# Performance work log

Measured on AMD Instinct MI355X. Metric: run time of the kernel, lower is better.

The kernel has to match this reference:

```python
import jax, jax.numpy as jnp
import numpy as np

N = 20000
E = 320000
IN_C = 256
OUT_C = 64
HEADS = 4
NEG_SLOPE = 0.2
HID = HEADS * OUT_C  # 256, layer-2 input width (concat=True)


def setup_inputs() -> dict:
    key = jax.random.key(0)
    ks = jax.random.split(key, 16)
    x = jax.random.normal(ks[0], (N, IN_C), dtype=jnp.float32)
    edge_index = jax.random.randint(ks[1], (2, E), 0, N, dtype=jnp.int32)

    def glorot(k, shape, fan_in):
        return jax.random.normal(k, shape, dtype=jnp.float32) * np.float32(1.0 / np.sqrt(fan_in))

    inp = {"x": x, "edge_index": edge_index}
    # two GATv2Conv layers, both in_dim=256 -> heads*out=256
    for li, kbase in ((1, 2), (2, 9)):
        in_dim = IN_C if li == 1 else HID
        inp[f"Wl{li}"] = glorot(ks[kbase + 0], (in_dim, HID), in_dim)
        inp[f"bl{li}"] = jnp.zeros((HID,), jnp.float32)
        inp[f"Wr{li}"] = glorot(ks[kbase + 1], (in_dim, HID), in_dim)
        inp[f"br{li}"] = jnp.zeros((HID,), jnp.float32)
        inp[f"att{li}"] = glorot(ks[kbase + 2], (HEADS, OUT_C), OUT_C)
        inp[f"bias{li}"] = jnp.zeros((HID,), jnp.float32)
    return inp


def _gatv2_layer(x, src, dst, Wl, bl, Wr, br, att, bias):
    # GATv2Conv (PyG semantics, eval mode so attention dropout is identity)
    xl = (x @ Wl + bl).reshape(N, HEADS, OUT_C)  # source transform
    xr = (x @ Wr + br).reshape(N, HEADS, OUT_C)  # target transform
    # per-edge attention logits: a^T LeakyReLU(xl_j + xr_i)
    e = jax.nn.leaky_relu(xl[src] + xr[dst], NEG_SLOPE)      # [E2, H, C]
    logits = jnp.einsum('ehc,hc->eh', e, att)                # [E2, H]
    # segment softmax over incoming edges of each target node
    m = jax.ops.segment_max(logits, dst, num_segments=N)      # [N, H]
    ex = jnp.exp(logits - m[dst])
    denom = jax.ops.segment_sum(ex, dst, num_segments=N)      # [N, H]
    alpha = ex / denom[dst]                                   # [E2, H]
    msg = xl[src] * alpha[:, :, None]                         # [E2, H, C]
    out = jax.ops.segment_sum(msg, dst, num_segments=N)       # [N, H, C]
    return out.reshape(N, HID) + bias


def reference(x, edge_index, Wl1, bl1, Wr1, br1, att1, bias1,
              Wl2, bl2, Wr2, br2, att2, bias2):
    # add self loops (PyG GATv2Conv default add_self_loops=True)
    loops = jnp.arange(N, dtype=edge_index.dtype)
    src = jnp.concatenate([edge_index[0], loops])
    dst = jnp.concatenate([edge_index[1], loops])
    h = _gatv2_layer(x, src, dst, Wl1, bl1, Wr1, br1, att1, bias1)
    h = jax.nn.relu(h)
    h = _gatv2_layer(h, src, dst, Wl2, bl2, Wr2, br2, att2, bias2)
    h = jax.nn.relu(h)
    return h
```

## Files before the change

### kernel.cpp

```cpp
#include <hip/hip_runtime.h>

#define N_NODES 20000
#define E_EDGES 320000
#define E2 (E_EDGES + N_NODES)
#define HID 256
#define SLOPE 0.2f

typedef __bf16 bf16x8 __attribute__((ext_vector_type(8)));
typedef float  f32x4  __attribute__((ext_vector_type(4)));
typedef unsigned int uint4v __attribute__((ext_vector_type(4)));

__device__ __forceinline__ unsigned short f2bf(float f) {
    unsigned b = __float_as_uint(f);
    return (unsigned short)((b + 0x7FFFu + ((b >> 16) & 1u)) >> 16);
}
__device__ __forceinline__ float bf2f(unsigned short h) {
    return __uint_as_float(((unsigned)h) << 16);
}
__device__ __forceinline__ bf16x8 ld_frag(const unsigned short* p) {
    uint4v u = *reinterpret_cast<const uint4v*>(p);
    return __builtin_bit_cast(bf16x8, u);
}
#define MFMA16(a, b, c) __builtin_amdgcn_mfma_f32_16x16x32_bf16((a), (b), (c), 0, 0, 0)

__global__ __launch_bounds__(256) void k_init(int* __restrict__ deg, int* __restrict__ cursor) {
    int i = blockIdx.x * 256 + threadIdx.x;
    if (i < N_NODES) { deg[i] = 1; cursor[i] = 0; }
}

__global__ __launch_bounds__(256) void k_degree(const int* __restrict__ dst, int* __restrict__ deg) {
    int e = blockIdx.x * 256 + threadIdx.x;
    if (e < E_EDGES) atomicAdd(&deg[dst[e]], 1);
}

__global__ __launch_bounds__(1024) void k_scan(const int* __restrict__ deg, int* __restrict__ off) {
    __shared__ int wsum[16];
    const int tid  = threadIdx.x;
    const int wave = tid >> 6;
    const int lane = tid & 63;
    int carry = 0;
    for (int base = 0; base < N_NODES; base += 1024) {
        const int i = base + tid;
        const int v = (i < N_NODES) ? deg[i] : 0;
        int x = v;
        #pragma unroll
        for (int o = 1; o < 64; o <<= 1) {
            int t = __shfl_up(x, o);
            if (lane >= o) x += t;
        }
        if (lane == 63) wsum[wave] = x;
        __syncthreads();
        if (wave == 0 && lane < 16) {
            int y = wsum[lane];
            #pragma unroll
            for (int o = 1; o < 16; o <<= 1) {
                int t = __shfl_up(y, o);
                if (lane >= o) y += t;
            }
            wsum[lane] = y;
        }
        __syncthreads();
        const int wbase = (wave == 0) ? 0 : wsum[wave - 1];
        if (i < N_NODES) off[i] = carry + wbase + (x - v);
        carry += wsum[15];
        __syncthreads();
    }
    if (tid == 0) off[N_NODES] = carry;
}

__global__ __launch_bounds__(256) void k_fill(const int* __restrict__ srcA, const int* __restrict__ dstA,
                                              const int* __restrict__ off, int* __restrict__ cursor,
                                              int* __restrict__ csr_src) {
    int e = blockIdx.x * 256 + threadIdx.x;
    if (e >= E2) return;
    int s, d;
    if (e < E_EDGES) { s = srcA[e]; d = dstA[e]; }
    else             { s = d = e - E_EDGES; }
    int pos = atomicAdd(&cursor[d], 1);
    csr_src[off[d] + pos] = s;
}

__global__ __launch_bounds__(256) void k_cvt_x(const float* __restrict__ X,
                                               unsigned short* __restrict__ hi,
                                               unsigned short* __restrict__ lo) {
    const int i = blockIdx.x * 256 + threadIdx.x;
    if (i >= N_NODES * HID / 4) return;
    float4 v = ((const float4*)X)[i];
    ushort4 h, l;
    h.x = f2bf(v.x); l.x = f2bf(v.x - bf2f(h.x));
    h.y = f2bf(v.y); l.y = f2bf(v.y - bf2f(h.y));
    h.z = f2bf(v.z); l.z = f2bf(v.z - bf2f(h.z));
    h.w = f2bf(v.w); l.w = f2bf(v.w - bf2f(h.w));
    ((ushort4*)hi)[i] = h;
    ((ushort4*)lo)[i] = l;
}

__global__ __launch_bounds__(256) void k_cvt_w(const float* __restrict__ W0, const float* __restrict__ W1,
                                               const float* __restrict__ W2, const float* __restrict__ W3,
                                               unsigned short* __restrict__ wt_hi,
                                               unsigned short* __restrict__ wt_lo) {
    const float* W = (blockIdx.x == 0) ? W0 : (blockIdx.x == 1) ? W1 : (blockIdx.x == 2) ? W2 : W3;
    unsigned short* oh = wt_hi + (size_t)blockIdx.x * 65536;
    unsigned short* ol = wt_lo + (size_t)blockIdx.x * 65536;
    const int n = threadIdx.x;
    const int k0 = blockIdx.y * 16;
    for (int k = k0; k < k0 + 16; ++k) {
        float v = W[(size_t)k * 256 + n];
        unsigned short h = f2bf(v);
        oh[(size_t)n * 256 + k] = h;
        ol[(size_t)n * 256 + k] = f2bf(v - bf2f(h));
    }
}

__global__ __launch_bounds__(256) void k_gemm_mfma(
        const unsigned short* __restrict__ Ahi, const unsigned short* __restrict__ Alo,
        const unsigned short* __restrict__ WhiL, const unsigned short* __restrict__ WloL,
        const unsigned short* __restrict__ WhiR, const unsigned short* __restrict__ WloR,
        const float* __restrict__ bl, const float* __restrict__ br,
        float* __restrict__ xl, float* __restrict__ xr) {
    const int tid  = threadIdx.x;
    const int lane = tid & 63;
    const int wave = tid >> 6;
    const int m0   = blockIdx.x * 128 + wave * 32;
    const int n0   = blockIdx.y * 64;

    const int lrow = lane & 15;
    const int lkb  = lane >> 4;
    int ar0 = m0 + lrow;       ar0 = (ar0 < N_NODES) ? ar0 : N_NODES - 1;
    int ar1 = m0 + 16 + lrow;  ar1 = (ar1 < N_NODES) ? ar1 : N_NODES - 1;
    const size_t aoff0 = (size_t)ar0 * HID + lkb * 8;
    const size_t aoff1 = (size_t)ar1 * HID + lkb * 8;

    f32x4 accL[2][4], accR[2][4];
    #pragma unroll
    for (int i = 0; i < 2; ++i)
        #pragma unroll
        for (int j = 0; j < 4; ++j) {
            accL[i][j] = (f32x4){0.f, 0.f, 0.f, 0.f};
            accR[i][j] = (f32x4){0.f, 0.f, 0.f, 0.f};
        }

    #pragma unroll
    for (int k0 = 0; k0 < 256; k0 += 32) {
        const bf16x8 a0h = ld_frag(Ahi + aoff0 + k0);
        const bf16x8 a0l = ld_frag(Alo + aoff0 + k0);
        const bf16x8 a1h = ld_frag(Ahi + aoff1 + k0);
        const bf16x8 a1l = ld_frag(Alo + aoff1 + k0);
        #pragma unroll
        for (int ct = 0; ct < 4; ++ct) {
            const size_t boff = (size_t)(n0 + ct * 16 + lrow) * HID + k0 + lkb * 8;
            const bf16x8 bhL = ld_frag(WhiL + boff);
            const bf16x8 blo = ld_frag(WloL + boff);
            const bf16x8 bhR = ld_frag(WhiR + boff);
            const bf16x8 brl = ld_frag(WloR + boff);
            accL[0][ct] = MFMA16(a0h, bhL, accL[0][ct]);
            accL[0][ct] = MFMA16(a0h, blo, accL[0][ct]);
            accL[0][ct] = MFMA16(a0l, bhL, accL[0][ct]);
            accL[1][ct] = MFMA16(a1h, bhL, accL[1][ct]);
            accL[1][ct] = MFMA16(a1h, blo, accL[1][ct]);
            accL[1][ct] = MFMA16(a1l, bhL, accL[1][ct]);
            accR[0][ct] = MFMA16(a0h, bhR, accR[0][ct]);
            accR[0][ct] = MFMA16(a0h, brl, accR[0][ct]);
            accR[0][ct] = MFMA16(a0l, bhR, accR[0][ct]);
            accR[1][ct] = MFMA16(a1h, bhR, accR[1][ct]);
            accR[1][ct] = MFMA16(a1h, brl, accR[1][ct]);
            accR[1][ct] = MFMA16(a1l, bhR, accR[1][ct]);
        }
    }

    #pragma unroll
    for (int ct = 0; ct < 4; ++ct) {
        const int gcol = n0 + ct * 16 + lrow;
        const float bbl = bl[gcol];
        const float bbr = br[gcol];
        #pragma unroll
        for (int rt = 0; rt < 2; ++rt) {
            #pragma unroll
            for (int j = 0; j < 4; ++j) {
                const int grow = m0 + rt * 16 + lkb * 4 + j;
                if (grow < N_NODES) {
                    xl[(size_t)grow * HID + gcol] = accL[rt][ct][j] + bbl;
                    xr[(size_t)grow * HID + gcol] = accR[rt][ct][j] + bbr;
                }
            }
        }
    }
}

template <bool FP32OUT>
__global__ __launch_bounds__(256) void k_edge(const float* __restrict__ xl, const float* __restrict__ xr,
                                              const float* __restrict__ att,
                                              const int* __restrict__ csr_src, const int* __restrict__ off,
                                              const float* __restrict__ bias,
                                              float* __restrict__ outF,
                                              unsigned short* __restrict__ outHi,
                                              unsigned short* __restrict__ outLo) {
    const int node = (blockIdx.x * 256 + threadIdx.x) >> 6;
    const int l = threadIdx.x & 63;
    if (node >= N_NODES) return;

    const float4 w  = *(const float4*)&att[l * 4];
    const float4 xd = *(const float4*)&xr[(size_t)node * 256 + l * 4];
    const int beg = off[node], end = off[node + 1];

    float m = -1e30f, ssum = 0.f;
    float4 acc = make_float4(0.f, 0.f, 0.f, 0.f);

    int j1 = csr_src[beg];
    float4 a_nxt = *(const float4*)&xl[(size_t)j1 * 256 + l * 4];
    int j2 = (beg + 1 < end) ? csr_src[beg + 1] : 0;

    for (int p = beg; p < end; ++p) {
        const float4 a = a_nxt;
        if (p + 1 < end)
            a_nxt = *(const float4*)&xl[(size_t)j2 * 256 + l * 4];
        if (p + 2 < end)
            j2 = csr_src[p + 2];

        float t = 0.f, u;
        u = a.x + xd.x; u = (u > 0.f) ? u : SLOPE * u; t = fmaf(u, w.x, t);
        u = a.y + xd.y; u = (u > 0.f) ? u : SLOPE * u; t = fmaf(u, w.y, t);
        u = a.z + xd.z; u = (u > 0.f) ? u : SLOPE * u; t = fmaf(u, w.z, t);
        u = a.w + xd.w; u = (u > 0.f) ? u : SLOPE * u; t = fmaf(u, w.w, t);
        t += __shfl_xor(t, 1);
        t += __shfl_xor(t, 2);
        t += __shfl_xor(t, 4);
        t += __shfl_xor(t, 8);

        const float nm = fmaxf(m, t);
        const float sc = __expf(m - nm);
        const float wp = __expf(t - nm);
        acc.x = fmaf(acc.x, sc, wp * a.x);
        acc.y = fmaf(acc.y, sc, wp * a.y);
        acc.z = fmaf(acc.z, sc, wp * a.z);
        acc.w = fmaf(acc.w, sc, wp * a.w);
        ssum  = fmaf(ssum, sc, wp);
        m = nm;
    }
    const float inv = 1.0f / ssum;
    const float4 bv = *(const float4*)&bias[l * 4];
    float4 o;
    o.x = fmaxf(fmaf(acc.x, inv, bv.x), 0.f);
    o.y = fmaxf(fmaf(acc.y, inv, bv.y), 0.f);
    o.z = fmaxf(fmaf(acc.z, inv, bv.z), 0.f);
    o.w = fmaxf(fmaf(acc.w, inv, bv.w), 0.f);
    if (FP32OUT) {
        *(float4*)&outF[(size_t)node * 256 + l * 4] = o;
    } else {
        ushort4 h, lo;
        h.x = f2bf(o.x); lo.x = f2bf(o.x - bf2f(h.x));
        h.y = f2bf(o.y); lo.y = f2bf(o.y - bf2f(h.y));
        h.z = f2bf(o.z); lo.z = f2bf(o.z - bf2f(h.z));
        h.w = f2bf(o.w); lo.w = f2bf(o.w - bf2f(h.w));
        *(ushort4*)&outHi[(size_t)node * 256 + l * 4] = h;
        *(ushort4*)&outLo[(size_t)node * 256 + l * 4] = lo;
    }
}

extern "C" void kernel_launch(void* const* d_in, const int* in_sizes, int n_in,
                              void* d_out, int out_size, void* d_ws, size_t ws_size,
                              hipStream_t stream) {
    const float* x    = (const float*)d_in[0];
    const int*   ei   = (const int*)d_in[1];
    const float* Wl1  = (const float*)d_in[2];
    const float* bl1  = (const float*)d_in[3];
    const float* Wr1  = (const float*)d_in[4];
    const float* br1  = (const float*)d_in[5];
    const float* att1 = (const float*)d_in[6];
    const float* bias1= (const float*)d_in[7];
    const float* Wl2  = (const float*)d_in[8];
    const float* bl2  = (const float*)d_in[9];
    const float* Wr2  = (const float*)d_in[10];
    const float* br2  = (const float*)d_in[11];
    const float* att2 = (const float*)d_in[12];
    const float* bias2= (const float*)d_in[13];
    float* out = (float*)d_out;

    const int* src = ei;
    const int* dst = ei + E_EDGES;

    char* ws = (char*)d_ws;
    size_t o = 0;
    auto alloc = [&](size_t bytes) -> void* {
        void* p = ws + o;
        o += (bytes + 255) & ~(size_t)255;
        return p;
    };
    float*          xl      = (float*)alloc((size_t)N_NODES * HID * 4);
    float*          xr      = (float*)alloc((size_t)N_NODES * HID * 4);
    unsigned short* bufA_hi = (unsigned short*)alloc((size_t)N_NODES * HID * 2);
    unsigned short* bufA_lo = (unsigned short*)alloc((size_t)N_NODES * HID * 2);
    unsigned short* wt_hi   = (unsigned short*)alloc((size_t)4 * 65536 * 2);
    unsigned short* wt_lo   = (unsigned short*)alloc((size_t)4 * 65536 * 2);
    int*            csr_src = (int*)alloc((size_t)E2 * 4);
    int*            off     = (int*)alloc((size_t)(N_NODES + 1) * 4);
    int*            deg     = (int*)alloc((size_t)N_NODES * 4);
    int*            cursor  = (int*)alloc((size_t)N_NODES * 4);
    (void)ws_size; (void)n_in; (void)in_sizes; (void)out_size;

    k_init<<<(N_NODES + 255) / 256, 256, 0, stream>>>(deg, cursor);
    k_degree<<<(E_EDGES + 255) / 256, 256, 0, stream>>>(dst, deg);
    k_scan<<<1, 1024, 0, stream>>>(deg, off);
    k_fill<<<(E2 + 255) / 256, 256, 0, stream>>>(src, dst, off, cursor, csr_src);

    k_cvt_w<<<dim3(4, 16), 256, 0, stream>>>(Wl1, Wr1, Wl2, Wr2, wt_hi, wt_lo);
    k_cvt_x<<<(N_NODES * HID / 4 + 255) / 256, 256, 0, stream>>>(x, bufA_hi, bufA_lo);

    dim3 ggrid((N_NODES + 127) / 128, 4);
    const int egrid = (N_NODES * 64 + 255) / 256;

    k_gemm_mfma<<<ggrid, 256, 0, stream>>>(bufA_hi, bufA_lo,
                                           wt_hi, wt_lo, wt_hi + 65536, wt_lo + 65536,
                                           bl1, br1, xl, xr);
    k_edge<false><<<egrid, 256, 0, stream>>>(xl, xr, att1, csr_src, off, bias1,
                                             nullptr, bufA_hi, bufA_lo);

    k_gemm_mfma<<<ggrid, 256, 0, stream>>>(bufA_hi, bufA_lo,
                                           wt_hi + 2 * 65536, wt_lo + 2 * 65536,
                                           wt_hi + 3 * 65536, wt_lo + 3 * 65536,
                                           bl2, br2, xl, xr);
    k_edge<true><<<egrid, 256, 0, stream>>>(xl, xr, att2, csr_src, off, bias2,
                                            out, nullptr, nullptr);
}
```

Before: 383.3 us.

## Split per-node edge softmax across four waves with LDS merge

The edge aggregation kernel now assigns one 256-thread block per node. Each of the four waves processes a strided subset of incoming edges with its own online softmax state. Partial max, sum and accumulator values are merged through shared memory before the output is written per channel. This shortens the serial per-node dependency chain, at the cost of a block barrier, LDS traffic and idle waves on low-degree nodes. The init kernel is replaced by memsets, with the self-loop degree folded into the scan.

```diff
diff --git a/kernel.cpp b/kernel.cpp
--- a/kernel.cpp
+++ b/kernel.cpp
@@ -22,11 +22,6 @@
     return __builtin_bit_cast(bf16x8, u);
 }
 #define MFMA16(a, b, c) __builtin_amdgcn_mfma_f32_16x16x32_bf16((a), (b), (c), 0, 0, 0)
-
-__global__ __launch_bounds__(256) void k_init(int* __restrict__ deg, int* __restrict__ cursor) {
-    int i = blockIdx.x * 256 + threadIdx.x;
-    if (i < N_NODES) { deg[i] = 1; cursor[i] = 0; }
-}
 
 __global__ __launch_bounds__(256) void k_degree(const int* __restrict__ dst, int* __restrict__ deg) {
     int e = blockIdx.x * 256 + threadIdx.x;
@@ -41,7 +36,7 @@
     int carry = 0;
     for (int base = 0; base < N_NODES; base += 1024) {
         const int i = base + tid;
-        const int v = (i < N_NODES) ? deg[i] : 0;
+        const int v = (i < N_NODES) ? (deg[i] + 1) : 0;
         int x = v;
         #pragma unroll
         for (int o = 1; o < 64; o <<= 1) {
@@ -195,33 +190,39 @@
                                               float* __restrict__ outF,
                                               unsigned short* __restrict__ outHi,
                                               unsigned short* __restrict__ outLo) {
-    const int node = (blockIdx.x * 256 + threadIdx.x) >> 6;
-    const int l = threadIdx.x & 63;
-    if (node >= N_NODES) return;
-
-    const float4 w  = *(const float4*)&att[l * 4];
+    __shared__ float mS[4][4];
+    __shared__ float sS[4][4];
+    __shared__ float accS[4][256];
+    const int node = blockIdx.x;
+    const int tid  = threadIdx.x;
+    const int w    = tid >> 6;
+    const int l    = tid & 63;
+    const int h    = l >> 4;
+
+    const float4 aw = *(const float4*)&att[l * 4];
     const float4 xd = *(const float4*)&xr[(size_t)node * 256 + l * 4];
     const int beg = off[node], end = off[node + 1];
 
     float m = -1e30f, ssum = 0.f;
     float4 acc = make_float4(0.f, 0.f, 0.f, 0.f);
 
-    int j1 = csr_src[beg];
-    float4 a_nxt = *(const float4*)&xl[(size_t)j1 * 256 + l * 4];
-    int j2 = (beg + 1 < end) ? csr_src[beg + 1] : 0;
-
-    for (int p = beg; p < end; ++p) {
+    int p = beg + w;
+    int jn = (p < end) ? csr_src[p] : 0;
+    float4 a_nxt = make_float4(0.f, 0.f, 0.f, 0.f);
+    if (p < end) a_nxt = *(const float4*)&xl[(size_t)jn * 256 + l * 4];
+
+    while (p < end) {
         const float4 a = a_nxt;
-        if (p + 1 < end)
-            a_nxt = *(const float4*)&xl[(size_t)j2 * 256 + l * 4];
-        if (p + 2 < end)
-            j2 = csr_src[p + 2];
-
+        const int pn = p + 4;
+        if (pn < end) {
+            jn = csr_src[pn];
+            a_nxt = *(const float4*)&xl[(size_t)jn * 256 + l * 4];
+        }
         float t = 0.f, u;
-        u = a.x + xd.x; u = (u > 0.f) ? u : SLOPE * u; t = fmaf(u, w.x, t);
-        u = a.y + xd.y; u = (u > 0.f) ? u : SLOPE * u; t = fmaf(u, w.y, t);
-        u = a.z + xd.z; u = (u > 0.f) ? u : SLOPE * u; t = fmaf(u, w.z, t);
-        u = a.w + xd.w; u = (u > 0.f) ? u : SLOPE * u; t = fmaf(u, w.w, t);
+        u = a.x + xd.x; u = (u > 0.f) ? u : SLOPE * u; t = fmaf(u, aw.x, t);
+        u = a.y + xd.y; u = (u > 0.f) ? u : SLOPE * u; t = fmaf(u, aw.y, t);
+        u = a.z + xd.z; u = (u > 0.f) ? u : SLOPE * u; t = fmaf(u, aw.z, t);
+        u = a.w + xd.w; u = (u > 0.f) ? u : SLOPE * u; t = fmaf(u, aw.w, t);
         t += __shfl_xor(t, 1);
         t += __shfl_xor(t, 2);
         t += __shfl_xor(t, 4);
@@ -236,24 +237,29 @@
         acc.w = fmaf(acc.w, sc, wp * a.w);
         ssum  = fmaf(ssum, sc, wp);
         m = nm;
-    }
-    const float inv = 1.0f / ssum;
-    const float4 bv = *(const float4*)&bias[l * 4];
-    float4 o;
-    o.x = fmaxf(fmaf(acc.x, inv, bv.x), 0.f);
-    o.y = fmaxf(fmaf(acc.y, inv, bv.y), 0.f);
-    o.z = fmaxf(fmaf(acc.z, inv, bv.z), 0.f);
-    o.w = fmaxf(fmaf(acc.w, inv, bv.w), 0.f);
+        p = pn;
+    }
+    if ((l & 15) == 0) { mS[w][h] = m; sS[w][h] = ssum; }
+    accS[w][l * 4 + 0] = acc.x;
+    accS[w][l * 4 + 1] = acc.y;
+    accS[w][l * 4 + 2] = acc.z;
+    accS[w][l * 4 + 3] = acc.w;
+    __syncthreads();
+
+    const int ch = tid;
+    const int hh = ch >> 6;
+    const float m0 = mS[0][hh], m1 = mS[1][hh], m2 = mS[2][hh], m3 = mS[3][hh];
+    const float M  = fmaxf(fmaxf(m0, m1), fmaxf(m2, m3));
+    const float f0 = __expf(m0 - M), f1 = __expf(m1 - M), f2 = __expf(m2 - M), f3 = __expf(m3 - M);
+    const float S  = sS[0][hh] * f0 + sS[1][hh] * f1 + sS[2][hh] * f2 + sS[3][hh] * f3;
+    const float v  = accS[0][ch] * f0 + accS[1][ch] * f1 + accS[2][ch] * f2 + accS[3][ch] * f3;
+    const float o  = fmaxf(v / S + bias[ch], 0.f);
     if (FP32OUT) {
-        *(float4*)&outF[(size_t)node * 256 + l * 4] = o;
+        outF[(size_t)node * 256 + ch] = o;
     } else {
-        ushort4 h, lo;
-        h.x = f2bf(o.x); lo.x = f2bf(o.x - bf2f(h.x));
-        h.y = f2bf(o.y); lo.y = f2bf(o.y - bf2f(h.y));
-        h.z = f2bf(o.z); lo.z = f2bf(o.z - bf2f(h.z));
-        h.w = f2bf(o.w); lo.w = f2bf(o.w - bf2f(h.w));
-        *(ushort4*)&outHi[(size_t)node * 256 + l * 4] = h;
-        *(ushort4*)&outLo[(size_t)node * 256 + l * 4] = lo;
+        const unsigned short hi = f2bf(o);
+        outHi[(size_t)node * 256 + ch] = hi;
+        outLo[(size_t)node * 256 + ch] = f2bf(o - bf2f(hi));
     }
 }
 
@@ -298,7 +304,8 @@
     int*            cursor  = (int*)alloc((size_t)N_NODES * 4);
     (void)ws_size; (void)n_in; (void)in_sizes; (void)out_size;
 
-    k_init<<<(N_NODES + 255) / 256, 256, 0, stream>>>(deg, cursor);
+    hipMemsetAsync(deg,    0, (size_t)N_NODES * 4, stream);
+    hipMemsetAsync(cursor, 0, (size_t)N_NODES * 4, stream);
     k_degree<<<(E_EDGES + 255) / 256, 256, 0, stream>>>(dst, deg);
     k_scan<<<1, 1024, 0, stream>>>(deg, off);
     k_fill<<<(E2 + 255) / 256, 256, 0, stream>>>(src, dst, off, cursor, csr_src);
@@ -307,18 +314,17 @@
     k_cvt_x<<<(N_NODES * HID / 4 + 255) / 256, 256, 0, stream>>>(x, bufA_hi, bufA_lo);
 
     dim3 ggrid((N_NODES + 127) / 128, 4);
-    const int egrid = (N_NODES * 64 + 255) / 256;
 
     k_gemm_mfma<<<ggrid, 256, 0, stream>>>(bufA_hi, bufA_lo,
                                            wt_hi, wt_lo, wt_hi + 65536, wt_lo + 65536,
                                            bl1, br1, xl, xr);
-    k_edge<false><<<egrid, 256, 0, stream>>>(xl, xr, att1, csr_src, off, bias1,
-                                             nullptr, bufA_hi, bufA_lo);
+    k_edge<false><<<N_NODES, 256, 0, stream>>>(xl, xr, att1, csr_src, off, bias1,
+                                               nullptr, bufA_hi, bufA_lo);
 
     k_gemm_mfma<<<ggrid, 256, 0, stream>>>(bufA_hi, bufA_lo,
                                            wt_hi + 2 * 65536, wt_lo + 2 * 65536,
                                            wt_hi + 3 * 65536, wt_lo + 3 * 65536,
                                            bl2, br2, xl, xr);
-    k_edge<true><<<egrid, 256, 0, stream>>>(xl, xr, att2, csr_src, off, bias2,
-                                            out, nullptr, nullptr);
-}
+    k_edge<true><<<N_NODES, 256, 0, stream>>>(xl, xr, att2, csr_src, off, bias2,
+                                              out, nullptr, nullptr);
+}
```

Result: no change. 390.2 us (+1.8%).
